# Optimization experiments

Measured on AMD Instinct MI355X. Metric: run time of the kernel, lower is better.

Reference implementation:

```python
import jax, jax.numpy as jnp
import numpy as np

N, E, F, H, C, B = 50000, 800000, 256, 256, 10, 64
BN_EPS = 1e-5
ATT_SLOPE = 0.2   # GATConv attention LeakyReLU
ACT_SLOPE = 0.01  # torch.nn.LeakyReLU default

def _leaky(x, slope):
    return jnp.where(x >= 0, x, slope * x)

def _gat_conv(x, src, dst, W, a_src, a_dst, b, n):
    # x:[N,Fin] -> h:[N,Fout]; single-head GATConv with self-loops already in (src,dst)
    h = x @ W
    e_src = h @ a_src  # [N]
    e_dst = h @ a_dst  # [N]
    e = _leaky(e_src[src] + e_dst[dst], ATT_SLOPE)  # [E]
    m = jax.ops.segment_max(e, dst, num_segments=n)
    ex = jnp.exp(e - m[dst])
    s = jax.ops.segment_sum(ex, dst, num_segments=n)
    alpha = ex / s[dst]
    out = jax.ops.segment_sum(alpha[:, None] * h[src], dst, num_segments=n)
    return out + b

def setup_inputs() -> dict:
    key = jax.random.key(0)
    ks = jax.random.split(key, 16)
    x = jax.random.normal(ks[0], (N, F), dtype=jnp.float32)
    edge_index = jax.random.randint(ks[1], (2, E), 0, N, dtype=jnp.int64)
    batch = jnp.sort(jax.random.randint(ks[2], (N,), 0, B, dtype=jnp.int64))
    sc = 0.05
    return {
        "x": x, "edge_index": edge_index, "batch": batch, "batch_size": B,
        "W1": jax.random.normal(ks[3], (F, H), jnp.float32) * sc,
        "a_src1": jax.random.normal(ks[4], (H,), jnp.float32) * sc,
        "a_dst1": jax.random.normal(ks[5], (H,), jnp.float32) * sc,
        "b1": jnp.zeros((H,), jnp.float32),
        "gamma": jnp.ones((H,), jnp.float32),
        "beta": jnp.zeros((H,), jnp.float32),
        "W2": jax.random.normal(ks[6], (H, H), jnp.float32) * sc,
        "a_src2": jax.random.normal(ks[7], (H,), jnp.float32) * sc,
        "a_dst2": jax.random.normal(ks[8], (H,), jnp.float32) * sc,
        "b2": jnp.zeros((H,), jnp.float32),
        "lw1": jax.random.normal(ks[9], (H, H), jnp.float32) * sc,
        "lb1": jnp.zeros((H,), jnp.float32),
        "lw2": jax.random.normal(ks[10], (H, C), jnp.float32) * sc,
        "lb2": jnp.zeros((C,), jnp.float32),
    }

def reference(x, edge_index, batch, batch_size, W1, a_src1, a_dst1, b1,
              gamma, beta, W2, a_src2, a_dst2, b2, lw1, lb1, lw2, lb2):
    n = x.shape[0]
    loops = jnp.arange(n, dtype=edge_index.dtype)
    src = jnp.concatenate([edge_index[0], loops])
    dst = jnp.concatenate([edge_index[1], loops])
    # conv1 + LeakyReLU + BatchNorm (batch statistics, biased var)
    h = _gat_conv(x, src, dst, W1, a_src1, a_dst1, b1, n)
    h = _leaky(h, ACT_SLOPE)
    mean = jnp.mean(h, axis=0)
    var = jnp.var(h, axis=0)
    h = (h - mean) * jax.lax.rsqrt(var + BN_EPS) * gamma + beta
    # conv2 + LeakyReLU
    h = _gat_conv(h, src, dst, W2, a_src2, a_dst2, b2, n)
    h = _leaky(h, ACT_SLOPE)
    # global mean pool over graphs
    sums = jax.ops.segment_sum(h, batch, num_segments=batch_size)
    cnt = jax.ops.segment_sum(jnp.ones((n,), h.dtype), batch, num_segments=batch_size)
    g = sums / jnp.maximum(cnt, 1.0)[:, None]
    # MLP head
    g = _leaky(g @ lw1 + lb1, ACT_SLOPE)
    return g @ lw2 + lb2
```

## Files before the change

kernel.cpp:

```cpp
#include <hip/hip_runtime.h>
#include <math.h>

#define N_NODES 50000
#define N_EDGES 800000
#define ETOT    (N_EDGES + N_NODES)
#define FDIM    256
#define HDIM    256
#define NGRAPH  64
#define C_OUT   10
#define BN_EPS  1e-5f
#define ATT_SLOPE 0.2f
#define ACT_SLOPE 0.01f

#define NBUCK   ((N_NODES + 15) / 16)
#define BCAP    512
#define SORT_NB 96
#define EPB     ((ETOT + SORT_NB - 1) / SORT_NB)

typedef __attribute__((ext_vector_type(8))) short bf16x8;
typedef __attribute__((ext_vector_type(4))) float f32x4;

__device__ __forceinline__ float leaky(float x, float s) { return x >= 0.f ? x : s * x; }

__device__ __forceinline__ float bf2f(unsigned short u) {
    return __uint_as_float((unsigned)u << 16);
}
__device__ __forceinline__ unsigned short f2bf(float f) {
    unsigned u = __float_as_uint(f);
    u += 0x7FFF + ((u >> 16) & 1);
    return (unsigned short)(u >> 16);
}
__device__ __forceinline__ float rlF(float a, int j) {
    return __uint_as_float(__builtin_amdgcn_readlane(__float_as_uint(a), j));
}

__device__ __forceinline__ void edge_sd(const int* __restrict__ ei, int e, int& s, int& d) {
    if (e < N_EDGES) { s = ei[e]; d = ei[N_EDGES + e]; }
    else             { s = e - N_EDGES; d = s; }
}

__global__ __launch_bounds__(256) void prep_w(const float* __restrict__ W1,
                                              const float* __restrict__ W2,
                                              unsigned short* __restrict__ Wt1,
                                              unsigned short* __restrict__ Wt2) {
    int wb = blockIdx.x;
    const float* W = (wb < 256) ? W1 : W2;
    unsigned short* Wt = (wb < 256) ? Wt1 : Wt2;
    int idx = (wb & 255) * 256 + threadIdx.x;
    int n = idx >> 8, k = idx & 255;
    Wt[idx] = f2bf(W[k * 256 + n]);
}

template<bool AFFINE, bool FROMF32>
__global__ __launch_bounds__(512) void gemm_bf16(const void* __restrict__ Avp,
                                                 const unsigned short* __restrict__ Bt,
                                                 const float* __restrict__ scale,
                                                 const float* __restrict__ shift,
                                                 const float* __restrict__ avs,
                                                 const float* __restrict__ avd,
                                                 float* __restrict__ es,
                                                 float* __restrict__ ed,
                                                 unsigned short* __restrict__ C, int M) {
    __shared__ unsigned short Al[128 * 64];
    __shared__ unsigned short Bl[256 * 64];
    __shared__ float lred[4][128][2];
    const int tid = threadIdx.x;
    const int lane = tid & 63;
    const int wid = tid >> 6;
    const int wm = wid >> 2, wn = wid & 3;
    const int row0 = blockIdx.x * 128;
    const int g = lane >> 4, rl = lane & 15;

    f32x4 acc[4][4];
    #pragma unroll
    for (int m = 0; m < 4; ++m)
        #pragma unroll
        for (int n = 0; n < 4; ++n)
            acc[m][n] = (f32x4){0.f, 0.f, 0.f, 0.f};

    for (int kk = 0; kk < 256; kk += 64) {
        #pragma unroll
        for (int j = 0; j < 2; ++j) {
            int idx = j * 512 + tid;
            int row = idx >> 3, chunk = idx & 7;
            int sc = chunk ^ (row & 7);
            int grow = row0 + row; if (grow >= M) grow = M - 1;
            uint4 av;
            if (FROMF32) {
                const float* Af = (const float*)Avp;
                float4 f0 = *(const float4*)&Af[(size_t)grow * 256 + kk + chunk * 8];
                float4 f1 = *(const float4*)&Af[(size_t)grow * 256 + kk + chunk * 8 + 4];
                unsigned short* p = (unsigned short*)&av;
                p[0] = f2bf(f0.x); p[1] = f2bf(f0.y); p[2] = f2bf(f0.z); p[3] = f2bf(f0.w);
                p[4] = f2bf(f1.x); p[5] = f2bf(f1.y); p[6] = f2bf(f1.z); p[7] = f2bf(f1.w);
            } else {
                const unsigned short* Ab = (const unsigned short*)Avp;
                av = *(const uint4*)&Ab[(size_t)grow * 256 + kk + chunk * 8];
                if (AFFINE) {
                    unsigned short* p = (unsigned short*)&av;
                    int c0 = kk + chunk * 8;
                    #pragma unroll
                    for (int q = 0; q < 8; ++q)
                        p[q] = f2bf(bf2f(p[q]) * scale[c0 + q] + shift[c0 + q]);
                }
            }
            *(uint4*)&Al[row * 64 + sc * 8] = av;
        }
        #pragma unroll
        for (int j = 0; j < 4; ++j) {
            int idx = j * 512 + tid;
            int col = idx >> 3, chunk = idx & 7;
            int sc = chunk ^ (col & 7);
            uint4 bv = *(const uint4*)&Bt[(size_t)col * 256 + kk + chunk * 8];
            *(uint4*)&Bl[col * 64 + sc * 8] = bv;
        }
        __syncthreads();
        #pragma unroll
        for (int ks = 0; ks < 2; ++ks) {
            bf16x8 af[4], bfr[4];
            int chunk = ks * 4 + g;
            #pragma unroll
            for (int m = 0; m < 4; ++m) {
                int row = wm * 64 + m * 16 + rl;
                int sc = chunk ^ (row & 7);
                af[m] = *(const bf16x8*)&Al[row * 64 + sc * 8];
            }
            #pragma unroll
            for (int n = 0; n < 4; ++n) {
                int col = wn * 64 + n * 16 + rl;
                int sc = chunk ^ (col & 7);
                bfr[n] = *(const bf16x8*)&Bl[col * 64 + sc * 8];
            }
            #pragma unroll
            for (int m = 0; m < 4; ++m)
                #pragma unroll
                for (int n = 0; n < 4; ++n)
                    acc[m][n] = __builtin_amdgcn_mfma_f32_16x16x32_bf16(af[m], bfr[n], acc[m][n], 0, 0, 0);
        }
        __syncthreads();
    }
    #pragma unroll
    for (int m = 0; m < 4; ++m) {
        #pragma unroll
        for (int n = 0; n < 4; ++n) {
            int col = wn * 64 + n * 16 + rl;
            #pragma unroll
            for (int r = 0; r < 4; ++r) {
                int row = row0 + wm * 64 + m * 16 + g * 4 + r;
                if (row < M) C[(size_t)row * 256 + col] = f2bf(acc[m][n][r]);
            }
        }
    }
    float as_[4], ad_[4];
    #pragma unroll
    for (int n = 0; n < 4; ++n) {
        int col = wn * 64 + n * 16 + rl;
        as_[n] = avs[col]; ad_[n] = avd[col];
    }
    #pragma unroll
    for (int m = 0; m < 4; ++m) {
        #pragma unroll
        for (int r = 0; r < 4; ++r) {
            float ps = 0.f, pd = 0.f;
            #pragma unroll
            for (int n = 0; n < 4; ++n) {
                float v = acc[m][n][r];
                ps += v * as_[n]; pd += v * ad_[n];
            }
            #pragma unroll
            for (int off = 1; off < 16; off <<= 1) {
                ps += __shfl_xor(ps, off);
                pd += __shfl_xor(pd, off);
            }
            if (rl == 0) {
                int lr = wm * 64 + m * 16 + g * 4 + r;
                lred[wn][lr][0] = ps;
                lred[wn][lr][1] = pd;
            }
        }
    }
    __syncthreads();
    if (tid < 128) {
        int row = row0 + tid;
        if (row < M) {
            es[row] = (lred[0][tid][0] + lred[1][tid][0]) + (lred[2][tid][0] + lred[3][tid][0]);
            ed[row] = (lred[0][tid][1] + lred[1][tid][1]) + (lred[2][tid][1] + lred[3][tid][1]);
        }
    }
}

__global__ __launch_bounds__(256) void count_k(const int* __restrict__ ei,
                                               int* __restrict__ hist2d) {
    __shared__ int lcnt[NBUCK];
    int t = threadIdx.x, blk = blockIdx.x;
    for (int i = t; i < NBUCK; i += 256) lcnt[i] = 0;
    __syncthreads();
    int e0 = blk * EPB, e1 = min(e0 + EPB, ETOT);
    for (int e = e0 + t; e < e1; e += 256) {
        int s, d; edge_sd(ei, e, s, d);
        atomicAdd(&lcnt[d >> 4], 1);
    }
    __syncthreads();
    int* outp = hist2d + blk * NBUCK;
    for (int i = t; i < NBUCK; i += 256) outp[i] = lcnt[i];
}

__global__ __launch_bounds__(256) void colscan_k(int* __restrict__ hist2d,
                                                 int* __restrict__ bcnt) {
    int col = blockIdx.x * 256 + threadIdx.x;
    if (col >= NBUCK) return;
    int run = 0;
    for (int b = 0; b < SORT_NB; ++b) {
        int idx = b * NBUCK + col;
        int c = hist2d[idx];
        hist2d[idx] = run;
        run += c;
    }
    bcnt[col] = run;
}

__global__ __launch_bounds__(256) void scan_buckets(const int* __restrict__ bcnt,
                                                    int* __restrict__ bbase,
                                                    int* __restrict__ row_ptr) {
    __shared__ int s[256];
    constexpr int PER = (NBUCK + 255) / 256;
    int t = threadIdx.x;
    int loc[PER];
    int sum = 0;
    #pragma unroll
    for (int i = 0; i < PER; ++i) {
        int idx = t * PER + i;
        loc[i] = sum;
        sum += (idx < NBUCK) ? bcnt[idx] : 0;
    }
    s[t] = sum;
    __syncthreads();
    #pragma unroll
    for (int off = 1; off < 256; off <<= 1) {
        int add = (t >= off) ? s[t - off] : 0;
        __syncthreads();
        s[t] += add;
        __syncthreads();
    }
    int base = (t > 0) ? s[t - 1] : 0;
    #pragma unroll
    for (int i = 0; i < PER; ++i) {
        int idx = t * PER + i;
        if (idx < NBUCK) bbase[idx] = base + loc[i];
    }
    if (t == 0) row_ptr[N_NODES] = ETOT;
}

__global__ __launch_bounds__(256) void scatter2_k(const int* __restrict__ ei,
                                                  const int* __restrict__ hist2d,
                                                  int* __restrict__ bstore) {
    __shared__ int lcur[NBUCK];
    __shared__ int lbase[NBUCK];
    int t = threadIdx.x, blk = blockIdx.x;
    const int* boff = hist2d + blk * NBUCK;
    for (int i = t; i < NBUCK; i += 256) { lcur[i] = 0; lbase[i] = boff[i]; }
    __syncthreads();
    int e0 = blk * EPB, e1 = min(e0 + EPB, ETOT);
    for (int e = e0 + t; e < e1; e += 256) {
        int s, d; edge_sd(ei, e, s, d);
        int b = d >> 4;
        int r = atomicAdd(&lcur[b], 1);
        int pos = lbase[b] + r;
        if (pos < BCAP) bstore[(size_t)b * BCAP + pos] = s | ((d & 15) << 16);
    }
}

__global__ __launch_bounds__(256) void place_k(const int* __restrict__ bcnt,
                                               const int* __restrict__ bbase,
                                               const int* __restrict__ bstore,
                                               int* __restrict__ row_ptr,
                                               int* __restrict__ csr_src) {
    __shared__ int h16[16], e16[16], c16[16];
    int b = blockIdx.x, t = threadIdx.x;
    if (t < 16) { h16[t] = 0; c16[t] = 0; }
    __syncthreads();
    int sz = bcnt[b]; if (sz > BCAP) sz = BCAP;
    int base = bbase[b];
    const int* bs = bstore + (size_t)b * BCAP;
    int v0 = -1, v1 = -1;
    if (t < sz)       { v0 = bs[t];       atomicAdd(&h16[v0 >> 16], 1); }
    if (t + 256 < sz) { v1 = bs[t + 256]; atomicAdd(&h16[v1 >> 16], 1); }
    __syncthreads();
    if (t == 0) {
        int run = 0;
        #pragma unroll
        for (int j = 0; j < 16; ++j) { e16[j] = run; run += h16[j]; }
    }
    __syncthreads();
    if (t < 16) {
        int d = b * 16 + t;
        if (d < N_NODES) row_ptr[d] = base + e16[t];
    }
    if (v0 >= 0) {
        int dl = v0 >> 16;
        int pos = base + e16[dl] + atomicAdd(&c16[dl], 1);
        csr_src[pos] = v0 & 0xFFFF;
    }
    if (v1 >= 0) {
        int dl = v1 >> 16;
        int pos = base + e16[dl] + atomicAdd(&c16[dl], 1);
        csr_src[pos] = v1 & 0xFFFF;
    }
}

__device__ __forceinline__ void gather4(const unsigned short* __restrict__ hl,
                                        float a, int src, int lim,
                                        float4& A0, float4& A1, float4& A2, float4& A3) {
    int j = 0;
    for (; j + 3 < lim; j += 4) {
        float w0 = rlF(a, j + 0), w1 = rlF(a, j + 1), w2 = rlF(a, j + 2), w3 = rlF(a, j + 3);
        int s0 = __builtin_amdgcn_readlane(src, j + 0);
        int s1 = __builtin_amdgcn_readlane(src, j + 1);
        int s2 = __builtin_amdgcn_readlane(src, j + 2);
        int s3 = __builtin_amdgcn_readlane(src, j + 3);
        ushort4 v0 = *(const ushort4*)&hl[(size_t)s0 * HDIM];
        ushort4 v1 = *(const ushort4*)&hl[(size_t)s1 * HDIM];
        ushort4 v2 = *(const ushort4*)&hl[(size_t)s2 * HDIM];
        ushort4 v3 = *(const ushort4*)&hl[(size_t)s3 * HDIM];
        A0.x += w0 * bf2f(v0.x); A0.y += w0 * bf2f(v0.y); A0.z += w0 * bf2f(v0.z); A0.w += w0 * bf2f(v0.w);
        A1.x += w1 * bf2f(v1.x); A1.y += w1 * bf2f(v1.y); A1.z += w1 * bf2f(v1.z); A1.w += w1 * bf2f(v1.w);
        A2.x += w2 * bf2f(v2.x); A2.y += w2 * bf2f(v2.y); A2.z += w2 * bf2f(v2.z); A2.w += w2 * bf2f(v2.w);
        A3.x += w3 * bf2f(v3.x); A3.y += w3 * bf2f(v3.y); A3.z += w3 * bf2f(v3.z); A3.w += w3 * bf2f(v3.w);
    }
    for (; j < lim; ++j) {
        float w = rlF(a, j);
        int s = __builtin_amdgcn_readlane(src, j);
        ushort4 v = *(const ushort4*)&hl[(size_t)s * HDIM];
        A0.x += w * bf2f(v.x); A0.y += w * bf2f(v.y); A0.z += w * bf2f(v.z); A0.w += w * bf2f(v.w);
    }
}

__global__ __launch_bounds__(256) void dst_agg(const int* __restrict__ row_ptr,
                                               const int* __restrict__ csr_src,
                                               const float* __restrict__ es,
                                               const float* __restrict__ ed,
                                               const unsigned short* __restrict__ h,
                                               const float* __restrict__ bias,
                                               unsigned short* __restrict__ outb) {
    int d = blockIdx.x * 4 + (threadIdx.x >> 6);
    int lane = threadIdx.x & 63;
    if (d >= N_NODES) return;
    float4 b4 = *(const float4*)&bias[lane * 4];
    int start = row_ptr[d], end = row_ptr[d + 1];
    int deg = end - start;
    float edv = ed[d];
    const unsigned short* hl = h + lane * 4;
    float4 A0 = {0,0,0,0}, A1 = {0,0,0,0}, A2 = {0,0,0,0}, A3 = {0,0,0,0};
    float ssum = 0.f;

    if (deg > 0 && deg <= 64) {
        int src = 0; float v = -INFINITY;
        if (lane < deg) {
            src = csr_src[start + lane];
            v = leaky(es[src] + edv, ATT_SLOPE);
        }
        float m = v;
        #pragma unroll
        for (int off = 32; off; off >>= 1) m = fmaxf(m, __shfl_xor(m, off));
        float a = (lane < deg) ? expf(v - m) : 0.f;
        ssum = a;
        gather4(hl, a, src, deg, A0, A1, A2, A3);
    } else if (deg > 64) {
        float m = -INFINITY;
        for (int base = start; base < end; base += 64) {
            int idx = base + lane;
            if (idx < end) m = fmaxf(m, leaky(es[csr_src[idx]] + edv, ATT_SLOPE));
        }
        #pragma unroll
        for (int off = 32; off; off >>= 1) m = fmaxf(m, __shfl_xor(m, off));
        for (int base = start; base < end; base += 64) {
            int idx = base + lane;
            int src = 0; float a = 0.f;
            if (idx < end) {
                src = csr_src[idx];
                a = expf(leaky(es[src] + edv, ATT_SLOPE) - m);
            }
            ssum += a;
            int lim = end - base; if (lim > 64) lim = 64;
            gather4(hl, a, src, lim, A0, A1, A2, A3);
        }
    } else {
        ssum = 1.f;
    }
    #pragma unroll
    for (int off = 32; off; off >>= 1) ssum += __shfl_xor(ssum, off);
    float inv = (deg > 0) ? (1.f / ssum) : 0.f;
    float4 acc;
    acc.x = (A0.x + A1.x) + (A2.x + A3.x);
    acc.y = (A0.y + A1.y) + (A2.y + A3.y);
    acc.z = (A0.z + A1.z) + (A2.z + A3.z);
    acc.w = (A0.w + A1.w) + (A2.w + A3.w);
    ushort4 o;
    o.x = f2bf(leaky(acc.x * inv + b4.x, ACT_SLOPE));
    o.y = f2bf(leaky(acc.y * inv + b4.y, ACT_SLOPE));
    o.z = f2bf(leaky(acc.z * inv + b4.z, ACT_SLOPE));
    o.w = f2bf(leaky(acc.w * inv + b4.w, ACT_SLOPE));
    *(ushort4*)&outb[(size_t)d * HDIM + lane * 4] = o;
}

__global__ __launch_bounds__(256) void bn_stats_k(const unsigned short* __restrict__ buf,
                                                  float* __restrict__ csum,
                                                  float* __restrict__ csq) {
    int t = threadIdx.x;
    int rows_per = (N_NODES + gridDim.x - 1) / gridDim.x;
    int r0 = blockIdx.x * rows_per;
    int r1 = min(r0 + rows_per, N_NODES);
    float sum = 0.f, sq = 0.f;
    for (int r = r0; r < r1; ++r) {
        float v = bf2f(buf[(size_t)r * HDIM + t]);
        sum += v; sq += v * v;
    }
    atomicAdd(&csum[t], sum);
    atomicAdd(&csq[t], sq);
}

__global__ __launch_bounds__(256) void bn_param(const float* __restrict__ csum,
                                                const float* __restrict__ csq,
                                                const float* __restrict__ gamma,
                                                const float* __restrict__ beta,
                                                float* __restrict__ scale,
                                                float* __restrict__ shift) {
    int t = threadIdx.x;
    float mean = csum[t] / (float)N_NODES;
    float var = csq[t] / (float)N_NODES - mean * mean;
    float sc = gamma[t] * rsqrtf(var + BN_EPS);
    scale[t] = sc;
    shift[t] = beta[t] - mean * sc;
}

__global__ __launch_bounds__(256) void post_pool(const unsigned short* __restrict__ buf,
                                                 const int* __restrict__ batch,
                                                 float* __restrict__ gsum,
                                                 float* __restrict__ gcnt) {
    int t = threadIdx.x;
    int rows_per = (N_NODES + gridDim.x - 1) / gridDim.x;
    int r0 = blockIdx.x * rows_per;
    int r1 = min(r0 + rows_per, N_NODES);
    if (r0 >= r1) return;
    int curb = -1; float acc = 0.f; int cnt = 0;
    for (int r = r0; r < r1; ++r) {
        int bb = batch[r];
        if (bb != curb) {
            if (curb >= 0) {
                atomicAdd(&gsum[(size_t)curb * HDIM + t], acc);
                if (t == 0) atomicAdd(&gcnt[curb], (float)cnt);
            }
            curb = bb; acc = 0.f; cnt = 0;
        }
        acc += bf2f(buf[(size_t)r * HDIM + t]);
        cnt++;
    }
    if (curb >= 0) {
        atomicAdd(&gsum[(size_t)curb * HDIM + t], acc);
        if (t == 0) atomicAdd(&gcnt[curb], (float)cnt);
    }
}

__global__ __launch_bounds__(256) void mlp_head(const float* __restrict__ gsum,
                                                const float* __restrict__ gcnt,
                                                const float* __restrict__ lw1,
                                                const float* __restrict__ lb1,
                                                const float* __restrict__ lw2,
                                                const float* __restrict__ lb2,
                                                float* __restrict__ out) {
    __shared__ float g[HDIM];
    __shared__ float hid[HDIM];
    int b = blockIdx.x, t = threadIdx.x;
    float cnt = fmaxf(gcnt[b], 1.f);
    g[t] = gsum[(size_t)b * HDIM + t] / cnt;
    __syncthreads();
    float acc = lb1[t];
    for (int k = 0; k < HDIM; ++k) acc += g[k] * lw1[(size_t)k * HDIM + t];
    hid[t] = leaky(acc, ACT_SLOPE);
    __syncthreads();
    if (t < C_OUT) {
        float o = lb2[t];
        for (int k = 0; k < HDIM; ++k) o += hid[k] * lw2[(size_t)k * C_OUT + t];
        out[(size_t)b * C_OUT + t] = o;
    }
}

extern "C" void kernel_launch(void* const* d_in, const int* in_sizes, int n_in,
                              void* d_out, int out_size, void* d_ws, size_t ws_size,
                              hipStream_t stream) {
    const float* x      = (const float*)d_in[0];
    const int*   ei     = (const int*)d_in[1];
    const int*   batch  = (const int*)d_in[2];
    const float* W1     = (const float*)d_in[4];
    const float* a_src1 = (const float*)d_in[5];
    const float* a_dst1 = (const float*)d_in[6];
    const float* b1     = (const float*)d_in[7];
    const float* gamma  = (const float*)d_in[8];
    const float* beta   = (const float*)d_in[9];
    const float* W2     = (const float*)d_in[10];
    const float* a_src2 = (const float*)d_in[11];
    const float* a_dst2 = (const float*)d_in[12];
    const float* b2     = (const float*)d_in[13];
    const float* lw1    = (const float*)d_in[14];
    const float* lb1    = (const float*)d_in[15];
    const float* lw2    = (const float*)d_in[16];
    const float* lb2    = (const float*)d_in[17];
    float* out = (float*)d_out;

    const size_t NH = (size_t)N_NODES * HDIM;
    char* ws = (char*)d_ws;
    unsigned short* hbf     = (unsigned short*)ws; ws += NH * 2;
    unsigned short* aggbf   = (unsigned short*)ws; ws += NH * 2;
    unsigned short* Wt1     = (unsigned short*)ws; ws += 65536 * 2;
    unsigned short* Wt2     = (unsigned short*)ws; ws += 65536 * 2;
    float* es      = (float*)ws; ws += N_NODES * 4;
    float* ed      = (float*)ws; ws += N_NODES * 4;
    float* csum    = (float*)ws; ws += HDIM * 4;
    float* csq     = (float*)ws; ws += HDIM * 4;
    float* scale   = (float*)ws; ws += HDIM * 4;
    float* shift   = (float*)ws; ws += HDIM * 4;
    float* gsum    = (float*)ws; ws += NGRAPH * HDIM * 4;
    float* gcnt    = (float*)ws; ws += NGRAPH * 4;
    int*   row_ptr = (int*)ws;   ws += (N_NODES + 1) * 4;
    int*   bcnt    = (int*)ws;   ws += NBUCK * 4;
    int*   bbase   = (int*)ws;   ws += NBUCK * 4;
    int*   hist2d  = (int*)ws;   ws += (size_t)SORT_NB * NBUCK * 4;
    int*   csr_src = (int*)ws;   ws += (size_t)ETOT * 4;
    int*   bstore  = (int*)ws;   ws += (size_t)NBUCK * BCAP * 4;

    const int wave4_blocks = (N_NODES + 3) / 4;
    const int gemm_blocks = (N_NODES + 127) / 128;

    count_k<<<SORT_NB, 256, 0, stream>>>(ei, hist2d);
    colscan_k<<<(NBUCK + 255) / 256, 256, 0, stream>>>(hist2d, bcnt);
    scan_buckets<<<1, 256, 0, stream>>>(bcnt, bbase, row_ptr);
    scatter2_k<<<SORT_NB, 256, 0, stream>>>(ei, hist2d, bstore);
    place_k<<<NBUCK, 256, 0, stream>>>(bcnt, bbase, bstore, row_ptr, csr_src);

    prep_w<<<512, 256, 0, stream>>>(W1, W2, Wt1, Wt2);

    gemm_bf16<false, true><<<gemm_blocks, 512, 0, stream>>>(x, Wt1, nullptr, nullptr,
                                                            a_src1, a_dst1, es, ed, hbf, N_NODES);
    dst_agg<<<wave4_blocks, 256, 0, stream>>>(row_ptr, csr_src, es, ed, hbf, b1, aggbf);

    hipMemsetAsync(csum, 0, HDIM * 8, stream);
    bn_stats_k<<<256, 256, 0, stream>>>(aggbf, csum, csq);
    bn_param<<<1, 256, 0, stream>>>(csum, csq, gamma, beta, scale, shift);

    gemm_bf16<true, false><<<gemm_blocks, 512, 0, stream>>>(aggbf, Wt2, scale, shift,
                                                            a_src2, a_dst2, es, ed, hbf, N_NODES);
    dst_agg<<<wave4_blocks, 256, 0, stream>>>(row_ptr, csr_src, es, ed, hbf, b2, aggbf);

    hipMemsetAsync(gsum, 0, (size_t)(NGRAPH * HDIM + NGRAPH) * 4, stream);
    post_pool<<<256, 256, 0, stream>>>(aggbf, batch, gsum, gcnt);

    mlp_head<<<NGRAPH, 256, 0, stream>>>(gsum, gcnt, lw1, lb1, lw2, lb2, out);
}
```

Measured before the change: 342.0 us.

## Fold BatchNorm affine into W2 and use direct global-to-LDS loads in GEMM

Folds the BatchNorm scale into a new bf16 copy of W2 and its shift into a per-column bias, computed by a small fold_bn kernel. This drops the per-element affine transform from the second GEMM's A-tile loads. The bf16 A and B tiles are now loaded with global_load_lds straight into LDS instead of going through registers. Sort blocks are doubled and the count kernel reads only dst. The trade-offs are an extra tiny kernel launch and slightly different rounding, since scale is applied to the weights rather than the activations.

```diff
diff --git a/kernel.cpp b/kernel.cpp
--- a/kernel.cpp
+++ b/kernel.cpp
@@ -14,7 +14,7 @@
 
 #define NBUCK   ((N_NODES + 15) / 16)
 #define BCAP    512
-#define SORT_NB 96
+#define SORT_NB 192
 #define EPB     ((ETOT + SORT_NB - 1) / SORT_NB)
 
 typedef __attribute__((ext_vector_type(8))) short bf16x8;
@@ -32,6 +32,11 @@
 }
 __device__ __forceinline__ float rlF(float a, int j) {
     return __uint_as_float(__builtin_amdgcn_readlane(__float_as_uint(a), j));
+}
+
+__device__ __forceinline__ void gload_lds16(const unsigned short* g, unsigned short* l) {
+    __builtin_amdgcn_global_load_lds((const __attribute__((address_space(1))) void*)(g),
+                                     (__attribute__((address_space(3))) void*)(l), 16, 0, 0);
 }
 
 __device__ __forceinline__ void edge_sd(const int* __restrict__ ei, int e, int& s, int& d) {
@@ -51,11 +56,29 @@
     Wt[idx] = f2bf(W[k * 256 + n]);
 }
 
-template<bool AFFINE, bool FROMF32>
+__global__ __launch_bounds__(256) void fold_bn(const float* __restrict__ W2,
+                                               const float* __restrict__ scale,
+                                               const float* __restrict__ shift,
+                                               unsigned short* __restrict__ Wt2f,
+                                               float* __restrict__ cbias) {
+    __shared__ float red[256];
+    int n = blockIdx.x, k = threadIdx.x;
+    float w = W2[k * 256 + n];
+    Wt2f[n * 256 + k] = f2bf(w * scale[k]);
+    red[k] = w * shift[k];
+    __syncthreads();
+    #pragma unroll
+    for (int off = 128; off; off >>= 1) {
+        if (k < off) red[k] += red[k + off];
+        __syncthreads();
+    }
+    if (k == 0) cbias[n] = red[0];
+}
+
+template<bool FROMF32>
 __global__ __launch_bounds__(512) void gemm_bf16(const void* __restrict__ Avp,
                                                  const unsigned short* __restrict__ Bt,
-                                                 const float* __restrict__ scale,
-                                                 const float* __restrict__ shift,
+                                                 const float* __restrict__ cbias,
                                                  const float* __restrict__ avs,
                                                  const float* __restrict__ avd,
                                                  float* __restrict__ es,
@@ -79,40 +102,39 @@
             acc[m][n] = (f32x4){0.f, 0.f, 0.f, 0.f};
 
     for (int kk = 0; kk < 256; kk += 64) {
-        #pragma unroll
-        for (int j = 0; j < 2; ++j) {
-            int idx = j * 512 + tid;
-            int row = idx >> 3, chunk = idx & 7;
-            int sc = chunk ^ (row & 7);
-            int grow = row0 + row; if (grow >= M) grow = M - 1;
-            uint4 av;
-            if (FROMF32) {
-                const float* Af = (const float*)Avp;
+        if (FROMF32) {
+            const float* Af = (const float*)Avp;
+            #pragma unroll
+            for (int j = 0; j < 2; ++j) {
+                int idx = j * 512 + tid;
+                int row = idx >> 3, chunk = idx & 7;
+                int sc = chunk ^ (row & 7);
+                int grow = row0 + row; if (grow >= M) grow = M - 1;
                 float4 f0 = *(const float4*)&Af[(size_t)grow * 256 + kk + chunk * 8];
                 float4 f1 = *(const float4*)&Af[(size_t)grow * 256 + kk + chunk * 8 + 4];
+                uint4 av;
                 unsigned short* p = (unsigned short*)&av;
                 p[0] = f2bf(f0.x); p[1] = f2bf(f0.y); p[2] = f2bf(f0.z); p[3] = f2bf(f0.w);
                 p[4] = f2bf(f1.x); p[5] = f2bf(f1.y); p[6] = f2bf(f1.z); p[7] = f2bf(f1.w);
-            } else {
-                const unsigned short* Ab = (const unsigned short*)Avp;
-                av = *(const uint4*)&Ab[(size_t)grow * 256 + kk + chunk * 8];
-                if (AFFINE) {
-                    unsigned short* p = (unsigned short*)&av;
-                    int c0 = kk + chunk * 8;
-                    #pragma unroll
-                    for (int q = 0; q < 8; ++q)
-                        p[q] = f2bf(bf2f(p[q]) * scale[c0 + q] + shift[c0 + q]);
-                }
-            }
-            *(uint4*)&Al[row * 64 + sc * 8] = av;
+                *(uint4*)&Al[row * 64 + sc * 8] = av;
+            }
+        } else {
+            const unsigned short* Ab = (const unsigned short*)Avp;
+            #pragma unroll
+            for (int j = 0; j < 2; ++j) {
+                int rowBase = (j * 8 + wid) * 8;
+                int row = rowBase + (lane >> 3);
+                int grow = row0 + row; if (grow >= M) grow = M - 1;
+                int chunk = (lane & 7) ^ (row & 7);
+                gload_lds16(&Ab[(size_t)grow * 256 + kk + chunk * 8], &Al[rowBase * 64]);
+            }
         }
         #pragma unroll
         for (int j = 0; j < 4; ++j) {
-            int idx = j * 512 + tid;
-            int col = idx >> 3, chunk = idx & 7;
-            int sc = chunk ^ (col & 7);
-            uint4 bv = *(const uint4*)&Bt[(size_t)col * 256 + kk + chunk * 8];
-            *(uint4*)&Bl[col * 64 + sc * 8] = bv;
+            int colBase = (j * 8 + wid) * 8;
+            int col = colBase + (lane >> 3);
+            int chunk = (lane & 7) ^ (col & 7);
+            gload_lds16(&Bt[(size_t)col * 256 + kk + chunk * 8], &Bl[colBase * 64]);
         }
         __syncthreads();
         #pragma unroll
@@ -138,6 +160,17 @@
                     acc[m][n] = __builtin_amdgcn_mfma_f32_16x16x32_bf16(af[m], bfr[n], acc[m][n], 0, 0, 0);
         }
         __syncthreads();
+    }
+    if (cbias != nullptr) {
+        #pragma unroll
+        for (int n = 0; n < 4; ++n) {
+            float cb = cbias[wn * 64 + n * 16 + rl];
+            #pragma unroll
+            for (int m = 0; m < 4; ++m)
+                #pragma unroll
+                for (int r = 0; r < 4; ++r)
+                    acc[m][n][r] += cb;
+        }
     }
     #pragma unroll
     for (int m = 0; m < 4; ++m) {
@@ -197,7 +230,7 @@
     __syncthreads();
     int e0 = blk * EPB, e1 = min(e0 + EPB, ETOT);
     for (int e = e0 + t; e < e1; e += 256) {
-        int s, d; edge_sd(ei, e, s, d);
+        int d = (e < N_EDGES) ? ei[N_EDGES + e] : (e - N_EDGES);
         atomicAdd(&lcnt[d >> 4], 1);
     }
     __syncthreads();
@@ -513,12 +546,14 @@
     unsigned short* aggbf   = (unsigned short*)ws; ws += NH * 2;
     unsigned short* Wt1     = (unsigned short*)ws; ws += 65536 * 2;
     unsigned short* Wt2     = (unsigned short*)ws; ws += 65536 * 2;
+    unsigned short* Wt2f    = (unsigned short*)ws; ws += 65536 * 2;
     float* es      = (float*)ws; ws += N_NODES * 4;
     float* ed      = (float*)ws; ws += N_NODES * 4;
     float* csum    = (float*)ws; ws += HDIM * 4;
     float* csq     = (float*)ws; ws += HDIM * 4;
     float* scale   = (float*)ws; ws += HDIM * 4;
     float* shift   = (float*)ws; ws += HDIM * 4;
+    float* cbias   = (float*)ws; ws += HDIM * 4;
     float* gsum    = (float*)ws; ws += NGRAPH * HDIM * 4;
     float* gcnt    = (float*)ws; ws += NGRAPH * 4;
     int*   row_ptr = (int*)ws;   ws += (N_NODES + 1) * 4;
@@ -539,16 +574,17 @@
 
     prep_w<<<512, 256, 0, stream>>>(W1, W2, Wt1, Wt2);
 
-    gemm_bf16<false, true><<<gemm_blocks, 512, 0, stream>>>(x, Wt1, nullptr, nullptr,
-                                                            a_src1, a_dst1, es, ed, hbf, N_NODES);
+    gemm_bf16<true><<<gemm_blocks, 512, 0, stream>>>(x, Wt1, nullptr,
+                                                     a_src1, a_dst1, es, ed, hbf, N_NODES);
     dst_agg<<<wave4_blocks, 256, 0, stream>>>(row_ptr, csr_src, es, ed, hbf, b1, aggbf);
 
     hipMemsetAsync(csum, 0, HDIM * 8, stream);
     bn_stats_k<<<256, 256, 0, stream>>>(aggbf, csum, csq);
     bn_param<<<1, 256, 0, stream>>>(csum, csq, gamma, beta, scale, shift);
-
-    gemm_bf16<true, false><<<gemm_blocks, 512, 0, stream>>>(aggbf, Wt2, scale, shift,
-                                                            a_src2, a_dst2, es, ed, hbf, N_NODES);
+    fold_bn<<<256, 256, 0, stream>>>(W2, scale, shift, Wt2f, cbias);
+
+    gemm_bf16<false><<<gemm_blocks, 512, 0, stream>>>(aggbf, Wt2f, cbias,
+                                                      a_src2, a_dst2, es, ed, hbf, N_NODES);
     dst_agg<<<wave4_blocks, 256, 0, stream>>>(row_ptr, csr_src, es, ed, hbf, b2, aggbf);
 
     hipMemsetAsync(gsum, 0, (size_t)(NGRAPH * HDIM + NGRAPH) * 4, stream);
```

Measured after the change: 333.3 us. -2.5%, faster.
